# Optimization experiments

Hardware: AMD Instinct MI355X
Metric: run time of the kernel (lower is better)

The kernel has to match this reference:

```python
import jax, jax.numpy as jnp
import numpy as np

BLOCK_SIZE = 16
MASK_TOKEN_ID = 31999
D_MODEL = 2048
N_HEADS = 16
VOCAB = 32000
NEG = -1e30


def setup_inputs() -> dict:
    key = jax.random.key(0)
    ks = jax.random.split(key, 8)
    B, S, D, V = 1, 1024, D_MODEL, VOCAB
    sd = 1.0 / np.sqrt(D)
    return {
        "input_ids": jax.random.randint(ks[0], (B, S), 0, V),
        "attention_mask": jnp.ones((B, S), dtype=jnp.float32),
        "hidden_states": jax.random.normal(ks[1], (B, S, D), dtype=jnp.float32),
        "loss_mask": jnp.ones((B, S), dtype=jnp.float32),
        "embed_table": jax.random.normal(ks[2], (V, D), dtype=jnp.float32) * 0.02,
        "Wq": jax.random.normal(ks[3], (D, D), dtype=jnp.float32) * sd,
        "Wk": jax.random.normal(ks[4], (D, D), dtype=jnp.float32) * sd,
        "Wv": jax.random.normal(ks[5], (D, D), dtype=jnp.float32) * sd,
        "Wo": jax.random.normal(ks[6], (D, D), dtype=jnp.float32) * sd,
        "lm_head_w": jax.random.normal(ks[7], (D, V), dtype=jnp.float32) * sd,
    }


def reference(input_ids, attention_mask, hidden_states, loss_mask,
              embed_table, Wq, Wk, Wv, Wo, lm_head_w):
    B, S = input_ids.shape
    bs = BLOCK_SIZE
    L = (S // bs) * bs  # effective_len
    input_ids = input_ids[:, :L]
    hidden_states = hidden_states[:, :L, :]
    loss_mask = loss_mask[:, :L]

    positions = jnp.arange(L)
    is_block_start = positions % bs == 0
    block_ids = positions // bs

    # noise input: first token of each block real, rest MASK
    noise_ids = jnp.where(is_block_start[None, :], input_ids, MASK_TOKEN_ID)
    noise_emb = embed_table[noise_ids]  # [B, L, D]

    # [L, 2L] DFlash mask: ctx kv visible if its block < q block; noise kv if same block
    ctx_vis = block_ids[None, :] < block_ids[:, None]
    noise_vis = block_ids[:, None] == block_ids[None, :]
    full_mask = jnp.concatenate([ctx_vis, noise_vis], axis=1)  # [L, 2L] bool

    # draft attention: q from noise tokens, kv over [target_hidden ; noise]
    H = N_HEADS
    hd = hidden_states.shape[-1] // H
    kv_in = jnp.concatenate([hidden_states, noise_emb], axis=1)  # [B, 2L, D]
    q = (noise_emb @ Wq).reshape(B, L, H, hd).transpose(0, 2, 1, 3)      # [B,H,L,hd]
    k = (kv_in @ Wk).reshape(B, 2 * L, H, hd).transpose(0, 2, 1, 3)      # [B,H,2L,hd]
    v = (kv_in @ Wv).reshape(B, 2 * L, H, hd).transpose(0, 2, 1, 3)
    scores = jnp.einsum("bhqd,bhkd->bhqk", q, k) / jnp.sqrt(jnp.float32(hd))
    scores = jnp.where(full_mask[None, None, :, :], scores, NEG)
    attn = jax.nn.softmax(scores, axis=-1)
    ctx = jnp.einsum("bhqk,bhkd->bhqd", attn, v)
    hidden = ctx.transpose(0, 2, 1, 3).reshape(B, L, -1) @ Wo  # [B, L, D]

    logits = hidden @ lm_head_w  # [B, L, V]

    # dflash loss mask: exclude first block and block starts (gamma=None)
    is_first_block = block_ids == 0
    valid = (~is_first_block) & (~is_block_start)
    combined = loss_mask * valid.astype(jnp.float32)  # [B, L]
    active = combined > 1e-6

    logp = jax.nn.log_softmax(logits, axis=-1)
    ce = -jnp.take_along_axis(logp, input_ids[..., None], axis=-1)[..., 0]  # [B, L]
    count = jnp.sum(active.astype(jnp.float32))
    loss = jnp.sum(jnp.where(active, ce, 0.0)) / count

    preds = jnp.argmax(logits, axis=-1)
    correct = jnp.sum(jnp.where(active, (preds == input_ids).astype(jnp.float32), 0.0))
    accuracy = correct / count
    return loss, accuracy
```

## Files before the change

### kernel.cpp

```cpp
#include <hip/hip_runtime.h>

typedef unsigned int uint32;
typedef unsigned short u16;
typedef __attribute__((ext_vector_type(8))) short bf16x8;
typedef __attribute__((ext_vector_type(4))) float f32x4;

__device__ __forceinline__ u16 f2b(float f) {
  uint32 u = __float_as_uint(f);
  u = (u + 0x7fffu + ((u >> 16) & 1u)) >> 16;
  return (u16)u;
}
__device__ __forceinline__ float b2f(u16 h) {
  return __uint_as_float(((uint32)h) << 16);
}
__device__ __forceinline__ void gl_lds16(const void* g, void* l) {
  typedef const __attribute__((address_space(1))) void* gp_t;
  typedef __attribute__((address_space(3))) void* lp_t;
  __builtin_amdgcn_global_load_lds((gp_t)g, (lp_t)l, 16, 0, 0);
}

#define L 1024
#define D 2048
#define NH 16
#define HD 128
#define VOCAB 32000
#define KV 2048
#define MASK_ID 31999

static constexpr long OFF_KV  = 0;
static constexpr long OFF_WTQ = OFF_KV  + 8388608;
static constexpr long OFF_WTK = OFF_WTQ + 8388608;
static constexpr long OFF_WTV = OFF_WTK + 8388608;
static constexpr long OFF_WTO = OFF_WTV + 8388608;
static constexpr long OFF_Q   = OFF_WTO + 8388608;
static constexpr long OFF_K   = OFF_Q   + 4194304;
static constexpr long OFF_VT  = OFF_K   + 8388608;
static constexpr long OFF_CTX = OFF_VT  + 8388608;
static constexpr long OFF_HID = OFF_CTX + 4194304;
static constexpr long OFF_LMT = OFF_HID + 4194304;
static constexpr long OFF_PM  = OFF_LMT + 131072000;
static constexpr long OFF_PS  = OFF_PM  + 524288;
static constexpr long OFF_PI  = OFF_PS  + 524288;
static constexpr long OFF_PT  = OFF_PI  + 524288;
static constexpr long OFF_ROW = OFF_PT  + 4096;
static constexpr long WS_NEED = OFF_ROW + 8192;

__device__ __forceinline__ void transpose128(float* tile, const float* __restrict__ W,
                                             u16* __restrict__ WT,
                                             int Kd, int Nd, int k0, int n0) {
  int t = threadIdx.x;
  int r = t >> 2, cq = (t & 3) * 4;
#pragma unroll
  for (int p = 0; p < 8; ++p) {
    int c = cq + p * 16;
    float4 v = *(const float4*)(W + (long)(k0 + r) * Nd + n0 + c);
    float* d = tile + r * 129 + c;
    d[0] = v.x; d[1] = v.y; d[2] = v.z; d[3] = v.w;
  }
  __syncthreads();
  int q = t & 15, nn0 = t >> 4;
#pragma unroll
  for (int p = 0; p < 4; ++p) {
    int nn = nn0 + p * 32;
    union { u16 v[8]; bf16x8 b; } u;
#pragma unroll
    for (int j = 0; j < 8; ++j) u.v[j] = f2b(tile[(q * 8 + j) * 129 + nn]);
    *(bf16x8*)(WT + (long)(n0 + nn) * Kd + k0 + q * 8) = u.b;
  }
}

__global__ __launch_bounds__(512) void mega1(const float* __restrict__ hs,
                                             const int* __restrict__ ids,
                                             const float* __restrict__ emb,
                                             u16* __restrict__ kv,
                                             const float* __restrict__ Wq, const float* __restrict__ Wk,
                                             const float* __restrict__ Wv, const float* __restrict__ Wo,
                                             u16* __restrict__ wtq, u16* __restrict__ wtk,
                                             u16* __restrict__ wtv, u16* __restrict__ wto) {
  __shared__ float tile[128 * 129];
  int bid = blockIdx.x;
  int t = threadIdx.x;
  if (bid < 512) {
    int r = bid * 4 + (t >> 7);
    int c0 = (t & 127) * 16;
    const float* src;
    if (r < L) {
      src = hs + (long)r * D;
    } else {
      int p = r - L;
      int id = ((p & 15) == 0) ? ids[p] : MASK_ID;
      src = emb + (long)id * D;
    }
    u16* dst = kv + (long)r * D + c0;
#pragma unroll
    for (int qy = 0; qy < 2; ++qy) {
      float4 a = *(const float4*)(src + c0 + qy * 8);
      float4 b = *(const float4*)(src + c0 + qy * 8 + 4);
      ushort4 o0, o1;
      o0.x = f2b(a.x); o0.y = f2b(a.y); o0.z = f2b(a.z); o0.w = f2b(a.w);
      o1.x = f2b(b.x); o1.y = f2b(b.y); o1.z = f2b(b.z); o1.w = f2b(b.w);
      *(ushort4*)(dst + qy * 8) = o0;
      *(ushort4*)(dst + qy * 8 + 4) = o1;
    }
  } else {
    int idx = bid - 512;
    int z = idx >> 8, tt = idx & 255;
    const float* W = (z == 0) ? Wq : (z == 1) ? Wk : (z == 2) ? Wv : Wo;
    u16* T = (z == 0) ? wtq : (z == 1) ? wtk : (z == 2) ? wtv : wto;
    transpose128(tile, W, T, D, D, (tt >> 4) * 128, (tt & 15) * 128);
  }
}

#define EPI_PLAIN 0
#define EPI_QKV 3
#define EPI_CE 4

template <int EPI>
__global__ __launch_bounds__(256) void gemm128(const u16* __restrict__ A, int lda, long aHead,
                                               const u16* __restrict__ BT, int ldb, long bHead,
                                               u16* __restrict__ C, int ldc, long cHead,
                                               int Kd) {
  __shared__ __align__(16) char lds[16384];
  char* a_lds = lds;
  char* b_lds = lds + 8192;
  int tid = threadIdx.x;
  int lane = tid & 63;
  int wave = tid >> 6;
  int wr = wave >> 1, wc = wave & 1;
  int h = blockIdx.z;
  long tm = (long)blockIdx.x * 128;
  long tn = (long)blockIdx.y * 128;
  const u16* Ap = A + (long)h * aHead + tm * lda;
  const u16* Bp = BT + (long)h * bHead + tn * ldb;

  int soff = tid * 16;
  int srow = soff >> 6;
  int scol = (soff & 63) >> 1;
  char* aldsb = a_lds + wave * 1024;
  char* bldsb = b_lds + wave * 1024;

  f32x4 acc[4][4];
#pragma unroll
  for (int i = 0; i < 4; ++i)
#pragma unroll
    for (int j = 0; j < 4; ++j) acc[i][j] = (f32x4){0.f, 0.f, 0.f, 0.f};

  for (int k0 = 0; k0 < Kd; k0 += 32) {
#pragma unroll
    for (int r = 0; r < 2; ++r) {
      gl_lds16(Ap + (long)(srow + r * 64) * lda + k0 + scol, aldsb + r * 4096);
      gl_lds16(Bp + (long)(srow + r * 64) * ldb + k0 + scol, bldsb + r * 4096);
    }
    __syncthreads();
    bf16x8 af[4], bfr[4];
    int ka = (lane >> 4) << 4;
#pragma unroll
    for (int mi = 0; mi < 4; ++mi)
      af[mi] = *(const bf16x8*)(a_lds + (wr * 64 + mi * 16 + (lane & 15)) * 64 + ka);
#pragma unroll
    for (int ni = 0; ni < 4; ++ni)
      bfr[ni] = *(const bf16x8*)(b_lds + (wc * 64 + ni * 16 + (lane & 15)) * 64 + ka);
#pragma unroll
    for (int mi = 0; mi < 4; ++mi)
#pragma unroll
      for (int ni = 0; ni < 4; ++ni)
        acc[mi][ni] = __builtin_amdgcn_mfma_f32_16x16x32_bf16(af[mi], bfr[ni], acc[mi][ni], 0, 0, 0);
    __syncthreads();
  }

  long crow0 = tm + wr * 64 + ((lane >> 4) << 2);
  int ccol0 = wc * 64 + (lane & 15);
  u16* Cp = C + (long)h * cHead;
#pragma unroll
  for (int mi = 0; mi < 4; ++mi) {
#pragma unroll
    for (int ni = 0; ni < 4; ++ni) {
      long col = tn + ccol0 + ni * 16;
#pragma unroll
      for (int j = 0; j < 4; ++j) {
        long row = crow0 + mi * 16 + j;
        Cp[row * ldc + col] = f2b(acc[mi][ni][j]);
      }
    }
  }
}

template <int EPI>
__device__ __forceinline__ void gemm256_body(char* lds, int wg,
                                             const u16* __restrict__ A, int lda,
                                             const u16* __restrict__ BT,
                                             int Kd, int mtiles,
                                             u16* __restrict__ Cq, u16* __restrict__ Ck,
                                             u16* __restrict__ Cv,
                                             const int* __restrict__ ids,
                                             float* __restrict__ PMAX, float* __restrict__ PSUM,
                                             int* __restrict__ PARGI, float* __restrict__ PTGT) {
  int tm, tn;
  if (EPI == EPI_QKV) {
    if (wg < 32) { tn = wg >> 2; tm = 4 + (wg & 3); }
    else { int e = wg - 32; tn = 8 + (e >> 3); tm = e & 7; }
  } else {
    tm = wg % mtiles; tn = wg / mtiles;
  }

  int tid = threadIdx.x, lane = tid & 63, w = tid >> 6;
  int wm = w >> 2, wn = w & 3;
  int lq = lane & 15, qq = lane >> 4;
  const char* Ap = (const char*)(A + (long)tm * 256 * lda);
  const char* Bp = (const char*)(BT + (long)tn * 256 * lda);
  int NT = Kd >> 6;
  int maxs = NT << 2;

  int swz = qq ^ ((lq >> 1) & 3);
  char* pA0 = lds + ((wm * 128 + lq) * 64 + (swz << 4));
  char* pA1 = pA0 + 65536;
  char* pB0 = lds + 32768 + ((wn * 64 + lq) * 64 + (swz << 4));
  char* pB1 = pB0 + 65536;
  int voff[2], lof[2];
#pragma unroll
  for (int l = 0; l < 2; ++l) {
    int o = tid * 16 + l * 8192;
    int rr = o >> 6;
    int ch = (o >> 4) & 3;
    int clog = ch ^ ((rr >> 1) & 3);
    voff[l] = (rr * lda + clog * 8) * 2;
    lof[l] = w * 1024 + l * 8192;
  }

  auto STAGE_SLOT = [&](int s) {
    if (s >= maxs) return;
    int tau = s >> 2, hh = s & 3;
    int kind = (hh & 1) ^ 1;
    int ks = hh >> 1;
    const char* src = kind ? Bp : Ap;
    long kb = (long)tau * 128 + ks * 64;
    char* dstb = lds + (tau & 1) * 65536 + kind * 32768 + ks * 16384;
#pragma unroll
    for (int l = 0; l < 2; ++l)
      gl_lds16(src + kb + voff[l], dstb + lof[l]);
  };

  f32x4 acc[8][4];
#pragma unroll
  for (int i = 0; i < 8; ++i)
#pragma unroll
    for (int j = 0; j < 4; ++j) acc[i][j] = (f32x4){0.f, 0.f, 0.f, 0.f};

  STAGE_SLOT(0); STAGE_SLOT(1); STAGE_SLOT(2); STAGE_SLOT(3);
  asm volatile("s_waitcnt vmcnt(4)" ::: "memory");
  STAGE_SLOT(4); STAGE_SLOT(5); STAGE_SLOT(6);
  asm volatile("s_waitcnt vmcnt(6)" ::: "memory");
  __builtin_amdgcn_s_barrier();
  __builtin_amdgcn_sched_barrier(0);

  bf16x8 bfr[4];

#define G256_PHASE(PA, PB, KS, MH, SLOT, WAITV)                                \
  {                                                                            \
    bf16x8 af[4];                                                              \
    if (MH == 0) {                                                             \
      bfr[0] = *(const bf16x8*)((PB) + (KS) * 16384 + 0 * 1024);               \
      bfr[1] = *(const bf16x8*)((PB) + (KS) * 16384 + 1 * 1024);               \
      bfr[2] = *(const bf16x8*)((PB) + (KS) * 16384 + 2 * 1024);               \
      bfr[3] = *(const bf16x8*)((PB) + (KS) * 16384 + 3 * 1024);               \
    }                                                                          \
    af[0] = *(const bf16x8*)((PA) + (KS) * 16384 + (MH * 4 + 0) * 1024);       \
    af[1] = *(const bf16x8*)((PA) + (KS) * 16384 + (MH * 4 + 1) * 1024);       \
    af[2] = *(const bf16x8*)((PA) + (KS) * 16384 + (MH * 4 + 2) * 1024);       \
    af[3] = *(const bf16x8*)((PA) + (KS) * 16384 + (MH * 4 + 3) * 1024);       \
    STAGE_SLOT(SLOT);                                                          \
    __builtin_amdgcn_sched_barrier(0);                                         \
    __builtin_amdgcn_s_barrier();                                              \
    asm volatile("s_waitcnt lgkmcnt(0)" ::: "memory");                         \
    __builtin_amdgcn_sched_barrier(0);                                         \
    __builtin_amdgcn_s_setprio(1);                                             \
    _Pragma("unroll")                                                          \
    for (int mi2 = 0; mi2 < 4; ++mi2)                                          \
      _Pragma("unroll")                                                        \
      for (int ni = 0; ni < 4; ++ni)                                           \
        acc[MH * 4 + mi2][ni] = __builtin_amdgcn_mfma_f32_16x16x32_bf16(       \
            af[mi2], bfr[ni], acc[MH * 4 + mi2][ni], 0, 0, 0);                 \
    __builtin_amdgcn_s_setprio(0);                                             \
    __builtin_amdgcn_sched_barrier(0);                                         \
    if (WAITV == 6) asm volatile("s_waitcnt vmcnt(6)" ::: "memory");           \
    else if (WAITV == 0) asm volatile("s_waitcnt vmcnt(0)" ::: "memory");      \
    __builtin_amdgcn_s_barrier();                                              \
    __builtin_amdgcn_sched_barrier(0);                                         \
  }

  for (int t = 0; t < NT; t += 2) {
    int s0 = 4 * t;
    int w4 = (t + 2 >= NT) ? 0 : 6;
    G256_PHASE(pA0, pB0, 0, 0, s0 + 7,  -1)
    G256_PHASE(pA0, pB0, 0, 1, s0 + 8,  -1)
    G256_PHASE(pA0, pB0, 1, 0, s0 + 9,  -1)
    G256_PHASE(pA0, pB0, 1, 1, s0 + 10, w4)
    G256_PHASE(pA1, pB1, 0, 0, s0 + 11, -1)
    G256_PHASE(pA1, pB1, 0, 1, s0 + 12, -1)
    G256_PHASE(pA1, pB1, 1, 0, s0 + 13, -1)
    G256_PHASE(pA1, pB1, 1, 1, s0 + 14, 6)
  }
#undef G256_PHASE

  if (EPI == EPI_CE) {
    __syncthreads();
    float* smax = (float*)lds;
    float* ssum = smax + 1024;
    int* sargi = (int*)(ssum + 1024);
#pragma unroll
    for (int mi = 0; mi < 8; ++mi) {
#pragma unroll
      for (int j = 0; j < 4; ++j) {
        int lrow = mi * 16 + qq * 4 + j;
        long grow = (long)tm * 256 + wm * 128 + lrow;
        int tgt = ids[grow];
        float v[4];
        float mx = -1e30f; int ai = 0;
#pragma unroll
        for (int ni = 0; ni < 4; ++ni) {
          v[ni] = acc[mi][ni][j];
          int col = tn * 256 + wn * 64 + ni * 16 + lq;
          if (col == tgt) PTGT[grow] = v[ni];
          if (v[ni] > mx) { mx = v[ni]; ai = col; }
        }
#pragma unroll
        for (int off = 1; off < 16; off <<= 1) {
          float om = __shfl_xor(mx, off);
          int oa = __shfl_xor(ai, off);
          if (om > mx || (om == mx && oa < ai)) { mx = om; ai = oa; }
        }
        float se = 0.f;
#pragma unroll
        for (int ni = 0; ni < 4; ++ni) se += __expf(v[ni] - mx);
#pragma unroll
        for (int off = 1; off < 16; off <<= 1) se += __shfl_xor(se, off);
        if (lq == 0) {
          int f = wm * 128 + lrow;
          smax[f * 4 + wn] = mx;
          ssum[f * 4 + wn] = se;
          sargi[f * 4 + wn] = ai;
        }
      }
    }
    __syncthreads();
    if (lane < 32) {
      int f = w * 32 + lane;
      float m_t = smax[f * 4]; int a_t = sargi[f * 4];
#pragma unroll
      for (int x = 1; x < 4; ++x) {
        float om = smax[f * 4 + x]; int oa = sargi[f * 4 + x];
        if (om > m_t || (om == m_t && oa < a_t)) { m_t = om; a_t = oa; }
      }
      float s_t = 0.f;
#pragma unroll
      for (int x = 0; x < 4; ++x) s_t += ssum[f * 4 + x] * __expf(smax[f * 4 + x] - m_t);
      long grow = (long)tm * 256 + f;
      PMAX[grow * 128 + tn] = m_t;
      PSUM[grow * 128 + tn] = s_t;
      PARGI[grow * 128 + tn] = a_t;
    }
    return;
  }

  long crow = (long)tm * 256 + wm * 128 + ((lane >> 4) << 2);
  long ccol = (long)tn * 256 + wn * 64 + lq;
#pragma unroll
  for (int mi = 0; mi < 8; ++mi)
#pragma unroll
    for (int ni = 0; ni < 4; ++ni)
#pragma unroll
      for (int j = 0; j < 4; ++j) {
        long row = crow + mi * 16 + j;
        long col = ccol + ni * 16;
        u16 val = f2b(acc[mi][ni][j]);
        if (col < 2048) {
          if (row >= 1024) Cq[(row - 1024) * D + col] = val;
        } else if (col < 4096) {
          Ck[row * D + (col - 2048)] = val;
        } else {
          Cv[(col - 4096) * KV + row] = val;
        }
      }
}

__global__ __launch_bounds__(512, 2) void mega2(const u16* __restrict__ kv,
                                                const u16* __restrict__ wtq,
                                                u16* __restrict__ qb, u16* __restrict__ kb,
                                                u16* __restrict__ vt,
                                                const float* __restrict__ Wlm,
                                                u16* __restrict__ lmt) {
  __shared__ __align__(16) char lds[131072];
  int bid = blockIdx.x;
  if (bid < 160) {
    int wg = (bid & 7) * 20 + (bid >> 3);
    gemm256_body<EPI_QKV>(lds, wg, kv, D, wtq, D, 0, qb, kb, vt,
                          nullptr, nullptr, nullptr, nullptr, nullptr);
  } else {
    for (int tile = bid - 160; tile < 4000; tile += 352) {
      int n0 = (tile % 250) * 128;
      int k0 = (tile / 250) * 128;
      transpose128((float*)lds, Wlm, lmt, D, VOCAB, k0, n0);
      __syncthreads();
    }
  }
}

__global__ __launch_bounds__(512, 2) void gemm256_ce(const u16* __restrict__ A,
                                                     const u16* __restrict__ BT,
                                                     const int* __restrict__ ids,
                                                     float* __restrict__ PMAX, float* __restrict__ PSUM,
                                                     int* __restrict__ PARGI, float* __restrict__ PTGT) {
  __shared__ __align__(16) char lds[131072];
  int nwg = gridDim.x;
  int orig = blockIdx.x;
  int q8 = nwg >> 3, r8 = nwg & 7;
  int xcd = orig & 7, idx = orig >> 3;
  int wg = (xcd < r8 ? xcd * (q8 + 1) : r8 * (q8 + 1) + (xcd - r8) * q8) + idx;
  gemm256_body<EPI_CE>(lds, wg, A, D, BT, D, 4, nullptr, nullptr, nullptr,
                       ids, PMAX, PSUM, PARGI, PTGT);
}

__global__ __launch_bounds__(256) void ce_combine(const float* __restrict__ PMAX,
                                                  const float* __restrict__ PSUM,
                                                  const int* __restrict__ PARGI,
                                                  const float* __restrict__ PTGT,
                                                  const int* __restrict__ ids,
                                                  float* __restrict__ rowbuf) {
  int row = blockIdx.x * 4 + (threadIdx.x >> 6);
  int lane = threadIdx.x & 63;
  const float* pm = PMAX + (long)row * 128;
  const float* ps = PSUM + (long)row * 128;
  const int* pi = PARGI + (long)row * 128;
  float m0 = (lane < 125) ? pm[lane] : -1e30f;
  int a0 = (lane < 125) ? pi[lane] : (1 << 30);
  float m1 = (lane + 64 < 125) ? pm[lane + 64] : -1e30f;
  int a1 = (lane + 64 < 125) ? pi[lane + 64] : (1 << 30);
  float mg = m0; int ag = a0;
  if (m1 > mg || (m1 == mg && a1 < ag)) { mg = m1; ag = a1; }
  for (int off = 1; off < 64; off <<= 1) {
    float om = __shfl_xor(mg, off);
    int oa = __shfl_xor(ag, off);
    if (om > mg || (om == mg && oa < ag)) { mg = om; ag = oa; }
  }
  float s = 0.f;
  if (lane < 125) s += ps[lane] * __expf(m0 - mg);
  if (lane + 64 < 125) s += ps[lane + 64] * __expf(m1 - mg);
  for (int off = 1; off < 64; off <<= 1) s += __shfl_xor(s, off);
  if (lane == 0) {
    rowbuf[row * 2] = mg + logf(s) - PTGT[row];
    rowbuf[row * 2 + 1] = (ag == ids[row]) ? 1.f : 0.f;
  }
}

__global__ __launch_bounds__(256) void flash_attn(const u16* __restrict__ qb,
                                                  const u16* __restrict__ kb,
                                                  const u16* __restrict__ vt,
                                                  u16* __restrict__ ctx) {
  int tid = threadIdx.x;
  int lane = tid & 63;
  int wid = blockIdx.x * 4 + (tid >> 6);
  int pairid = wid >> 1;
  int h = pairid >> 5;
  int pr = pairid & 31;
  int rb = (wid & 1) ? (63 - pr) : pr;
  int lq = lane & 15;
  int g = lane >> 4;
  const float scale = 0.08838834764831845f;

  const u16* qrow = qb + (long)(rb * 16 + lq) * D + h * HD + g * 8;
  bf16x8 qf[4];
#pragma unroll
  for (int c = 0; c < 4; ++c) qf[c] = *(const bf16x8*)(qrow + c * 32);

  f32x4 o[8];
#pragma unroll
  for (int i = 0; i < 8; ++i) o[i] = (f32x4){0.f, 0.f, 0.f, 0.f};
  float m = -1e30f, lsum = 0.f;

  int nb = rb + 1;
  for (int bp = 0; bp < nb; bp += 2) {
    bool validB = (bp + 1) < nb;
    int tokA = (bp < rb) ? bp * 16 : 1024 + rb * 16;
    int bB = bp + 1;
    int tokB = validB ? ((bB < rb) ? bB * 16 : 1024 + rb * 16) : tokA;

    f32x4 sA = (f32x4){0.f, 0.f, 0.f, 0.f};
    f32x4 sB = (f32x4){0.f, 0.f, 0.f, 0.f};
    const u16* ka = kb + (long)(tokA + lq) * D + h * HD + g * 8;
#pragma unroll
    for (int c = 0; c < 4; ++c) {
      bf16x8 kf = *(const bf16x8*)(ka + c * 32);
      sA = __builtin_amdgcn_mfma_f32_16x16x32_bf16(kf, qf[c], sA, 0, 0, 0);
    }
    if (validB) {
      const u16* kbp = kb + (long)(tokB + lq) * D + h * HD + g * 8;
#pragma unroll
      for (int c = 0; c < 4; ++c) {
        bf16x8 kf = *(const bf16x8*)(kbp + c * 32);
        sB = __builtin_amdgcn_mfma_f32_16x16x32_bf16(kf, qf[c], sB, 0, 0, 0);
      }
    }

    float s8[8];
#pragma unroll
    for (int j = 0; j < 4; ++j) s8[j] = sA[j] * scale;
#pragma unroll
    for (int j = 0; j < 4; ++j) s8[4 + j] = validB ? sB[j] * scale : -1e30f;
    float mx = s8[0];
#pragma unroll
    for (int j = 1; j < 8; ++j) mx = fmaxf(mx, s8[j]);
    mx = fmaxf(mx, __shfl_xor(mx, 16));
    mx = fmaxf(mx, __shfl_xor(mx, 32));
    float mn = fmaxf(m, mx);
    float sc_f = __expf(m - mn);
    m = mn;
    float p[8], ps = 0.f;
#pragma unroll
    for (int j = 0; j < 8; ++j) { p[j] = __expf(s8[j] - mn); ps += p[j]; }
    ps += __shfl_xor(ps, 16);
    ps += __shfl_xor(ps, 32);
    lsum = lsum * sc_f + ps;

    uint32 Aw0 = (uint32)f2b(p[0]) | ((uint32)f2b(p[1]) << 16);
    uint32 Aw1 = (uint32)f2b(p[2]) | ((uint32)f2b(p[3]) << 16);
    uint32 Bw0 = (uint32)f2b(p[4]) | ((uint32)f2b(p[5]) << 16);
    uint32 Bw1 = (uint32)f2b(p[6]) | ((uint32)f2b(p[7]) << 16);
    int s0 = (((2 * g) & 3) << 4) + lq;
    int s1 = (((2 * g + 1) & 3) << 4) + lq;
    uint32 a00 = (uint32)__shfl((int)Aw0, s0), a01 = (uint32)__shfl((int)Aw1, s0);
    uint32 a10 = (uint32)__shfl((int)Aw0, s1), a11 = (uint32)__shfl((int)Aw1, s1);
    uint32 b00 = (uint32)__shfl((int)Bw0, s0), b01 = (uint32)__shfl((int)Bw1, s0);
    uint32 b10 = (uint32)__shfl((int)Bw0, s1), b11 = (uint32)__shfl((int)Bw1, s1);
    union { uint32 u[4]; bf16x8 v; } pu;
    pu.u[0] = (g < 2) ? a00 : b00;
    pu.u[1] = (g < 2) ? a01 : b01;
    pu.u[2] = (g < 2) ? a10 : b10;
    pu.u[3] = (g < 2) ? a11 : b11;

#pragma unroll
    for (int nt = 0; nt < 8; ++nt)
#pragma unroll
      for (int j = 0; j < 4; ++j) o[nt][j] *= sc_f;
    int tok_g = (g < 2) ? (tokA + g * 8) : (tokB + (g - 2) * 8);
    const u16* vrow = vt + (long)(h * HD + lq) * KV + tok_g;
#pragma unroll
    for (int nt = 0; nt < 8; ++nt) {
      bf16x8 vf = *(const bf16x8*)(vrow + (long)nt * 16 * KV);
      o[nt] = __builtin_amdgcn_mfma_f32_16x16x32_bf16(vf, pu.v, o[nt], 0, 0, 0);
    }
  }

  float inv = 1.f / lsum;
  u16* cp = ctx + (long)(rb * 16 + lq) * D + h * HD + g * 4;
#pragma unroll
  for (int nt = 0; nt < 8; ++nt) {
    ushort4 st;
    st.x = f2b(o[nt][0] * inv); st.y = f2b(o[nt][1] * inv);
    st.z = f2b(o[nt][2] * inv); st.w = f2b(o[nt][3] * inv);
    *(ushort4*)(cp + nt * 16) = st;
  }
}

__global__ __launch_bounds__(256) void final_reduce(const float* __restrict__ rowbuf,
                                                    const float* __restrict__ loss_mask,
                                                    float* __restrict__ out) {
  int t = threadIdx.x;
  float ce = 0.f, cnt = 0.f, cor = 0.f;
  for (int r = t; r < L; r += 256) {
    bool valid = (r >= 16) && ((r & 15) != 0);
    float comb = loss_mask[r] * (valid ? 1.f : 0.f);
    if (comb > 1e-6f) {
      ce += rowbuf[r * 2];
      cor += rowbuf[r * 2 + 1];
      cnt += 1.f;
    }
  }
  for (int off = 1; off < 64; off <<= 1) {
    ce += __shfl_xor(ce, off);
    cnt += __shfl_xor(cnt, off);
    cor += __shfl_xor(cor, off);
  }
  __shared__ float s1[4], s2[4], s3[4];
  int lane = t & 63, w = t >> 6;
  if (lane == 0) { s1[w] = ce; s2[w] = cnt; s3[w] = cor; }
  __syncthreads();
  if (t == 0) {
    float C = s1[0] + s1[1] + s1[2] + s1[3];
    float N = s2[0] + s2[1] + s2[2] + s2[3];
    float R = s3[0] + s3[1] + s3[2] + s3[3];
    out[0] = C / N;
    out[1] = R / N;
  }
}

__global__ void ws_too_small(float* out, float mb) {
  if (threadIdx.x == 0) { out[0] = 1e6f + mb; out[1] = -1e6f; }
}

extern "C" void kernel_launch(void* const* d_in, const int* in_sizes, int n_in,
                              void* d_out, int out_size, void* d_ws, size_t ws_size,
                              hipStream_t stream) {
  const int* ids = (const int*)d_in[0];
  const float* hs = (const float*)d_in[2];
  const float* lmask = (const float*)d_in[3];
  const float* emb = (const float*)d_in[4];
  const float* Wq = (const float*)d_in[5];
  const float* Wk = (const float*)d_in[6];
  const float* Wv = (const float*)d_in[7];
  const float* Wo = (const float*)d_in[8];
  const float* Wlm = (const float*)d_in[9];
  float* out = (float*)d_out;
  char* ws = (char*)d_ws;

  if (ws_size < (size_t)WS_NEED) {
    ws_too_small<<<1, 64, 0, stream>>>(out, (float)(ws_size >> 20));
    return;
  }

  u16* kv  = (u16*)(ws + OFF_KV);
  u16* wtq = (u16*)(ws + OFF_WTQ);
  u16* wtk = (u16*)(ws + OFF_WTK);
  u16* wtv = (u16*)(ws + OFF_WTV);
  u16* wto = (u16*)(ws + OFF_WTO);
  u16* qb  = (u16*)(ws + OFF_Q);
  u16* kb  = (u16*)(ws + OFF_K);
  u16* vt  = (u16*)(ws + OFF_VT);
  u16* ctx = (u16*)(ws + OFF_CTX);
  u16* hid = (u16*)(ws + OFF_HID);
  u16* lmt = (u16*)(ws + OFF_LMT);
  float* PMAX = (float*)(ws + OFF_PM);
  float* PSUM = (float*)(ws + OFF_PS);
  int* PARGI = (int*)(ws + OFF_PI);
  float* PTGT = (float*)(ws + OFF_PT);
  float* rowbuf = (float*)(ws + OFF_ROW);

  mega1<<<dim3(1536), 512, 0, stream>>>(hs, ids, emb, kv, Wq, Wk, Wv, Wo,
                                        wtq, wtk, wtv, wto);
  mega2<<<dim3(512), 512, 0, stream>>>(kv, wtq, qb, kb, vt, Wlm, lmt);

  flash_attn<<<dim3(256), 256, 0, stream>>>(qb, kb, vt, ctx);

  gemm128<EPI_PLAIN><<<dim3(8, 16, 1), 256, 0, stream>>>(ctx, D, 0, wto, D, 0, hid, D, 0, D);

  gemm256_ce<<<dim3(500), 512, 0, stream>>>(hid, lmt, ids, PMAX, PSUM, PARGI, PTGT);

  ce_combine<<<256, 256, 0, stream>>>(PMAX, PSUM, PARGI, PTGT, ids, rowbuf);
  final_reduce<<<1, 256, 0, stream>>>(rowbuf, lmask, out);
}
```

Baseline: 439.6 us.

## Replace 256-tile pipelined LM-head GEMM with simple 128-tile GEMM plus CE epilogue

The LM-head cross-entropy GEMM now runs on the simple 128x128 single-buffered gemm128 kernel with a fused max/sum/argmax epilogue, replacing the heavily pipelined 256x256 kernel. Partial-stat buffers double to 250 column tiles per row, and ce_combine reduces 250 partials instead of 125. The grid grows from 500 to 2000 workgroups, trading per-tile reuse and software pipelining for more parallelism and lower LDS use. It risks more global traffic and no load/compute overlap in the largest GEMM.

```diff
diff --git a/kernel.cpp b/kernel.cpp
--- a/kernel.cpp
+++ b/kernel.cpp
@@ -39,9 +39,9 @@
 static constexpr long OFF_HID = OFF_CTX + 4194304;
 static constexpr long OFF_LMT = OFF_HID + 4194304;
 static constexpr long OFF_PM  = OFF_LMT + 131072000;
-static constexpr long OFF_PS  = OFF_PM  + 524288;
-static constexpr long OFF_PI  = OFF_PS  + 524288;
-static constexpr long OFF_PT  = OFF_PI  + 524288;
+static constexpr long OFF_PS  = OFF_PM  + 1048576;
+static constexpr long OFF_PI  = OFF_PS  + 1048576;
+static constexpr long OFF_PT  = OFF_PI  + 1048576;
 static constexpr long OFF_ROW = OFF_PT  + 4096;
 static constexpr long WS_NEED = OFF_ROW + 8192;
 
@@ -116,10 +116,13 @@
 #define EPI_CE 4
 
 template <int EPI>
-__global__ __launch_bounds__(256) void gemm128(const u16* __restrict__ A, int lda, long aHead,
-                                               const u16* __restrict__ BT, int ldb, long bHead,
-                                               u16* __restrict__ C, int ldc, long cHead,
-                                               int Kd) {
+__global__ __launch_bounds__(256) void gemm128(const u16* __restrict__ A, int lda,
+                                               const u16* __restrict__ BT, int ldb,
+                                               u16* __restrict__ C, int ldc,
+                                               int Kd,
+                                               const int* __restrict__ ids,
+                                               float* __restrict__ PMAX, float* __restrict__ PSUM,
+                                               int* __restrict__ PARGI, float* __restrict__ PTGT) {
   __shared__ __align__(16) char lds[16384];
   char* a_lds = lds;
   char* b_lds = lds + 8192;
@@ -127,11 +130,9 @@
   int lane = tid & 63;
   int wave = tid >> 6;
   int wr = wave >> 1, wc = wave & 1;
-  int h = blockIdx.z;
-  long tm = (long)blockIdx.x * 128;
-  long tn = (long)blockIdx.y * 128;
-  const u16* Ap = A + (long)h * aHead + tm * lda;
-  const u16* Bp = BT + (long)h * bHead + tn * ldb;
+  int tm = blockIdx.x, tn = blockIdx.y;
+  const u16* Ap = A + (long)tm * 128 * lda;
+  const u16* Bp = BT + (long)tn * 128 * ldb;
 
   int soff = tid * 16;
   int srow = soff >> 6;
@@ -145,6 +146,7 @@
 #pragma unroll
     for (int j = 0; j < 4; ++j) acc[i][j] = (f32x4){0.f, 0.f, 0.f, 0.f};
 
+  int lq = lane & 15, q = lane >> 4;
   for (int k0 = 0; k0 < Kd; k0 += 32) {
 #pragma unroll
     for (int r = 0; r < 2; ++r) {
@@ -153,13 +155,13 @@
     }
     __syncthreads();
     bf16x8 af[4], bfr[4];
-    int ka = (lane >> 4) << 4;
+    int ka = q << 4;
 #pragma unroll
     for (int mi = 0; mi < 4; ++mi)
-      af[mi] = *(const bf16x8*)(a_lds + (wr * 64 + mi * 16 + (lane & 15)) * 64 + ka);
+      af[mi] = *(const bf16x8*)(a_lds + (wr * 64 + mi * 16 + lq) * 64 + ka);
 #pragma unroll
     for (int ni = 0; ni < 4; ++ni)
-      bfr[ni] = *(const bf16x8*)(b_lds + (wc * 64 + ni * 16 + (lane & 15)) * 64 + ka);
+      bfr[ni] = *(const bf16x8*)(b_lds + (wc * 64 + ni * 16 + lq) * 64 + ka);
 #pragma unroll
     for (int mi = 0; mi < 4; ++mi)
 #pragma unroll
@@ -168,41 +170,82 @@
     __syncthreads();
   }
 
-  long crow0 = tm + wr * 64 + ((lane >> 4) << 2);
-  int ccol0 = wc * 64 + (lane & 15);
-  u16* Cp = C + (long)h * cHead;
+  if (EPI == EPI_CE) {
+    float* smax = (float*)lds;
+    float* ssum = smax + 256;
+    int* sargi = (int*)(ssum + 256);
+#pragma unroll
+    for (int mi = 0; mi < 4; ++mi) {
+#pragma unroll
+      for (int j = 0; j < 4; ++j) {
+        int lrow = wr * 64 + mi * 16 + q * 4 + j;
+        long grow = (long)tm * 128 + lrow;
+        int tgt = ids[grow];
+        float v[4];
+        float mx = -1e30f; int ai = 0;
+#pragma unroll
+        for (int ni = 0; ni < 4; ++ni) {
+          v[ni] = acc[mi][ni][j];
+          int col = tn * 128 + wc * 64 + ni * 16 + lq;
+          if (col == tgt) PTGT[grow] = v[ni];
+          if (v[ni] > mx) { mx = v[ni]; ai = col; }
+        }
+#pragma unroll
+        for (int off = 1; off < 16; off <<= 1) {
+          float om = __shfl_xor(mx, off);
+          int oa = __shfl_xor(ai, off);
+          if (om > mx || (om == mx && oa < ai)) { mx = om; ai = oa; }
+        }
+        float se = 0.f;
+#pragma unroll
+        for (int ni = 0; ni < 4; ++ni) se += __expf(v[ni] - mx);
+#pragma unroll
+        for (int off = 1; off < 16; off <<= 1) se += __shfl_xor(se, off);
+        if (lq == 0) {
+          smax[lrow * 2 + wc] = mx;
+          ssum[lrow * 2 + wc] = se;
+          sargi[lrow * 2 + wc] = ai;
+        }
+      }
+    }
+    __syncthreads();
+    if (tid < 128) {
+      int f = tid;
+      float m0 = smax[f * 2], m1 = smax[f * 2 + 1];
+      int a0 = sargi[f * 2], a1 = sargi[f * 2 + 1];
+      float mt = m0; int at = a0;
+      if (m1 > mt || (m1 == mt && a1 < at)) { mt = m1; at = a1; }
+      float st = ssum[f * 2] * __expf(m0 - mt) + ssum[f * 2 + 1] * __expf(m1 - mt);
+      long grow = (long)tm * 128 + f;
+      PMAX[grow * 256 + tn] = mt;
+      PSUM[grow * 256 + tn] = st;
+      PARGI[grow * 256 + tn] = at;
+    }
+    return;
+  }
+
+  long crow0 = (long)tm * 128 + wr * 64 + (q << 2);
+  int ccol0 = wc * 64 + lq;
 #pragma unroll
   for (int mi = 0; mi < 4; ++mi) {
 #pragma unroll
     for (int ni = 0; ni < 4; ++ni) {
-      long col = tn + ccol0 + ni * 16;
+      long col = (long)tn * 128 + ccol0 + ni * 16;
 #pragma unroll
       for (int j = 0; j < 4; ++j) {
         long row = crow0 + mi * 16 + j;
-        Cp[row * ldc + col] = f2b(acc[mi][ni][j]);
+        C[row * ldc + col] = f2b(acc[mi][ni][j]);
       }
     }
   }
 }
 
-template <int EPI>
-__device__ __forceinline__ void gemm256_body(char* lds, int wg,
-                                             const u16* __restrict__ A, int lda,
-                                             const u16* __restrict__ BT,
-                                             int Kd, int mtiles,
-                                             u16* __restrict__ Cq, u16* __restrict__ Ck,
-                                             u16* __restrict__ Cv,
-                                             const int* __restrict__ ids,
-                                             float* __restrict__ PMAX, float* __restrict__ PSUM,
-                                             int* __restrict__ PARGI, float* __restrict__ PTGT) {
-  int tm, tn;
-  if (EPI == EPI_QKV) {
-    if (wg < 32) { tn = wg >> 2; tm = 4 + (wg & 3); }
-    else { int e = wg - 32; tn = 8 + (e >> 3); tm = e & 7; }
-  } else {
-    tm = wg % mtiles; tn = wg / mtiles;
-  }
-
+__device__ __forceinline__ void gemm256_qkv(char* lds, int tm, int tn,
+                                            const u16* __restrict__ A, int lda,
+                                            const u16* __restrict__ BT,
+                                            int Kd,
+                                            u16* __restrict__ Cq, u16* __restrict__ Ck,
+                                            u16* __restrict__ Cv) {
   int tid = threadIdx.x, lane = tid & 63, w = tid >> 6;
   int wm = w >> 2, wn = w & 3;
   int lq = lane & 15, qq = lane >> 4;
@@ -302,66 +345,6 @@
   }
 #undef G256_PHASE
 
-  if (EPI == EPI_CE) {
-    __syncthreads();
-    float* smax = (float*)lds;
-    float* ssum = smax + 1024;
-    int* sargi = (int*)(ssum + 1024);
-#pragma unroll
-    for (int mi = 0; mi < 8; ++mi) {
-#pragma unroll
-      for (int j = 0; j < 4; ++j) {
-        int lrow = mi * 16 + qq * 4 + j;
-        long grow = (long)tm * 256 + wm * 128 + lrow;
-        int tgt = ids[grow];
-        float v[4];
-        float mx = -1e30f; int ai = 0;
-#pragma unroll
-        for (int ni = 0; ni < 4; ++ni) {
-          v[ni] = acc[mi][ni][j];
-          int col = tn * 256 + wn * 64 + ni * 16 + lq;
-          if (col == tgt) PTGT[grow] = v[ni];
-          if (v[ni] > mx) { mx = v[ni]; ai = col; }
-        }
-#pragma unroll
-        for (int off = 1; off < 16; off <<= 1) {
-          float om = __shfl_xor(mx, off);
-          int oa = __shfl_xor(ai, off);
-          if (om > mx || (om == mx && oa < ai)) { mx = om; ai = oa; }
-        }
-        float se = 0.f;
-#pragma unroll
-        for (int ni = 0; ni < 4; ++ni) se += __expf(v[ni] - mx);
-#pragma unroll
-        for (int off = 1; off < 16; off <<= 1) se += __shfl_xor(se, off);
-        if (lq == 0) {
-          int f = wm * 128 + lrow;
-          smax[f * 4 + wn] = mx;
-          ssum[f * 4 + wn] = se;
-          sargi[f * 4 + wn] = ai;
-        }
-      }
-    }
-    __syncthreads();
-    if (lane < 32) {
-      int f = w * 32 + lane;
-      float m_t = smax[f * 4]; int a_t = sargi[f * 4];
-#pragma unroll
-      for (int x = 1; x < 4; ++x) {
-        float om = smax[f * 4 + x]; int oa = sargi[f * 4 + x];
-        if (om > m_t || (om == m_t && oa < a_t)) { m_t = om; a_t = oa; }
-      }
-      float s_t = 0.f;
-#pragma unroll
-      for (int x = 0; x < 4; ++x) s_t += ssum[f * 4 + x] * __expf(smax[f * 4 + x] - m_t);
-      long grow = (long)tm * 256 + f;
-      PMAX[grow * 128 + tn] = m_t;
-      PSUM[grow * 128 + tn] = s_t;
-      PARGI[grow * 128 + tn] = a_t;
-    }
-    return;
-  }
-
   long crow = (long)tm * 256 + wm * 128 + ((lane >> 4) << 2);
   long ccol = (long)tn * 256 + wn * 64 + lq;
 #pragma unroll
@@ -393,8 +376,10 @@
   int bid = blockIdx.x;
   if (bid < 160) {
     int wg = (bid & 7) * 20 + (bid >> 3);
-    gemm256_body<EPI_QKV>(lds, wg, kv, D, wtq, D, 0, qb, kb, vt,
-                          nullptr, nullptr, nullptr, nullptr, nullptr);
+    int tm, tn;
+    if (wg < 32) { tn = wg >> 2; tm = 4 + (wg & 3); }
+    else { int e = wg - 32; tn = 8 + (e >> 3); tm = e & 7; }
+    gemm256_qkv(lds, tm, tn, kv, D, wtq, D, qb, kb, vt);
   } else {
     for (int tile = bid - 160; tile < 4000; tile += 352) {
       int n0 = (tile % 250) * 128;
@@ -403,21 +388,6 @@
       __syncthreads();
     }
   }
-}
-
-__global__ __launch_bounds__(512, 2) void gemm256_ce(const u16* __restrict__ A,
-                                                     const u16* __restrict__ BT,
-                                                     const int* __restrict__ ids,
-                                                     float* __restrict__ PMAX, float* __restrict__ PSUM,
-                                                     int* __restrict__ PARGI, float* __restrict__ PTGT) {
-  __shared__ __align__(16) char lds[131072];
-  int nwg = gridDim.x;
-  int orig = blockIdx.x;
-  int q8 = nwg >> 3, r8 = nwg & 7;
-  int xcd = orig & 7, idx = orig >> 3;
-  int wg = (xcd < r8 ? xcd * (q8 + 1) : r8 * (q8 + 1) + (xcd - r8) * q8) + idx;
-  gemm256_body<EPI_CE>(lds, wg, A, D, BT, D, 4, nullptr, nullptr, nullptr,
-                       ids, PMAX, PSUM, PARGI, PTGT);
 }
 
 __global__ __launch_bounds__(256) void ce_combine(const float* __restrict__ PMAX,
@@ -428,23 +398,28 @@
                                                   float* __restrict__ rowbuf) {
   int row = blockIdx.x * 4 + (threadIdx.x >> 6);
   int lane = threadIdx.x & 63;
-  const float* pm = PMAX + (long)row * 128;
-  const float* ps = PSUM + (long)row * 128;
-  const int* pi = PARGI + (long)row * 128;
-  float m0 = (lane < 125) ? pm[lane] : -1e30f;
-  int a0 = (lane < 125) ? pi[lane] : (1 << 30);
-  float m1 = (lane + 64 < 125) ? pm[lane + 64] : -1e30f;
-  int a1 = (lane + 64 < 125) ? pi[lane + 64] : (1 << 30);
-  float mg = m0; int ag = a0;
-  if (m1 > mg || (m1 == mg && a1 < ag)) { mg = m1; ag = a1; }
+  const float* pm = PMAX + (long)row * 256;
+  const float* ps = PSUM + (long)row * 256;
+  const int* pi = PARGI + (long)row * 256;
+  float lm[4]; int la[4]; float lsv[4];
+  float mg = -1e30f; int ag = (1 << 30);
+#pragma unroll
+  for (int s = 0; s < 4; ++s) {
+    int idx = lane + s * 64;
+    bool ok = idx < 250;
+    lm[s] = ok ? pm[idx] : -1e30f;
+    la[s] = ok ? pi[idx] : (1 << 30);
+    lsv[s] = ok ? ps[idx] : 0.f;
+    if (lm[s] > mg || (lm[s] == mg && la[s] < ag)) { mg = lm[s]; ag = la[s]; }
+  }
   for (int off = 1; off < 64; off <<= 1) {
     float om = __shfl_xor(mg, off);
     int oa = __shfl_xor(ag, off);
     if (om > mg || (om == mg && oa < ag)) { mg = om; ag = oa; }
   }
   float s = 0.f;
-  if (lane < 125) s += ps[lane] * __expf(m0 - mg);
-  if (lane + 64 < 125) s += ps[lane + 64] * __expf(m1 - mg);
+#pragma unroll
+  for (int x = 0; x < 4; ++x) s += lsv[x] * __expf(lm[x] - mg);
   for (int off = 1; off < 64; off <<= 1) s += __shfl_xor(s, off);
   if (lane == 0) {
     rowbuf[row * 2] = mg + logf(s) - PTGT[row];
@@ -640,9 +615,11 @@
 
   flash_attn<<<dim3(256), 256, 0, stream>>>(qb, kb, vt, ctx);
 
-  gemm128<EPI_PLAIN><<<dim3(8, 16, 1), 256, 0, stream>>>(ctx, D, 0, wto, D, 0, hid, D, 0, D);
-
-  gemm256_ce<<<dim3(500), 512, 0, stream>>>(hid, lmt, ids, PMAX, PSUM, PARGI, PTGT);
+  gemm128<EPI_PLAIN><<<dim3(8, 16), 256, 0, stream>>>(ctx, D, wto, D, hid, D, D,
+                                                      nullptr, nullptr, nullptr, nullptr, nullptr);
+
+  gemm128<EPI_CE><<<dim3(8, 250), 256, 0, stream>>>(hid, D, lmt, D, nullptr, 0, D,
+                                                    ids, PMAX, PSUM, PARGI, PTGT);
 
   ce_combine<<<256, 256, 0, stream>>>(PMAX, PSUM, PARGI, PTGT, ids, rowbuf);
   final_reduce<<<1, 256, 0, stream>>>(rowbuf, lmask, out);
```

Result: slower. 513.5 us (+16.8%).
